# Optimization experiments

Hardware: AMD Instinct MI355X
Metric: run time of the kernel (lower is better)

Reference implementation:

```python
import jax, jax.numpy as jnp
import numpy as np

RES = 32            # input grid resolution
OUT_RES = 64        # after subdivide
C = 128             # channels (== out_channels -> skip is identity)
G = 32              # group-norm groups
N = 8192            # active input voxels
EPS = 1e-5

# 8 child offsets for subdivide, 27 stencil offsets for 3x3x3 submanifold conv
_OFFS8 = np.stack(np.meshgrid([0, 1], [0, 1], [0, 1], indexing='ij'), -1).reshape(-1, 3).astype(np.int32)
_OFFS27 = np.stack(np.meshgrid([-1, 0, 1], [-1, 0, 1], [-1, 0, 1], indexing='ij'), -1).reshape(-1, 3).astype(np.int32)


def group_norm(x, gamma, beta, num_groups=G, eps=EPS):
    # sparse group norm over all active voxels of the (single) sample
    n, c = x.shape
    xg = x.reshape(n, num_groups, c // num_groups)
    mean = xg.mean(axis=(0, 2), keepdims=True)
    var = xg.var(axis=(0, 2), keepdims=True)
    xn = (xg - mean) * jax.lax.rsqrt(var + eps)
    return xn.reshape(n, c) * gamma + beta


def subdivide_coords(coords):
    offs = jnp.asarray(_OFFS8)
    return (coords[:, None, :] * 2 + offs[None, :, :]).reshape(-1, 3)  # [8N, 3]


def subm_conv3d(feats, coords, W, b, grid_res):
    # submanifold 3x3x3 sparse conv: outputs only at active sites
    n = feats.shape[0]
    grid = jnp.full((grid_res, grid_res, grid_res), -1, dtype=jnp.int32)
    grid = grid.at[coords[:, 0], coords[:, 1], coords[:, 2]].set(
        jnp.arange(n, dtype=jnp.int32))
    out = jnp.zeros((n, W.shape[-1]), dtype=feats.dtype)
    for k in range(27):  # fixed small stencil loop
        off = jnp.asarray(_OFFS27[k])
        nb = coords + off
        inb = jnp.all((nb >= 0) & (nb < grid_res), axis=1)
        nbc = jnp.clip(nb, 0, grid_res - 1)
        idx = grid[nbc[:, 0], nbc[:, 1], nbc[:, 2]]
        mask = inb & (idx >= 0)
        g = jnp.where(mask[:, None], feats[jnp.where(mask, idx, 0)], 0.0)
        out = out + g @ W[k]
    return out + b


def setup_inputs() -> dict:
    key = jax.random.key(0)
    ks = jax.random.split(key, 8)
    rng = np.random.default_rng(0)
    flat = rng.choice(RES ** 3, size=N, replace=False)
    coords = np.stack([flat // (RES * RES), (flat // RES) % RES, flat % RES],
                      axis=-1).astype(np.int32)
    feats = jax.random.normal(ks[0], (N, C), dtype=jnp.float32)
    gamma1 = 1.0 + 0.1 * jax.random.normal(ks[1], (C,), dtype=jnp.float32)
    beta1 = 0.1 * jax.random.normal(ks[2], (C,), dtype=jnp.float32)
    W1 = jax.random.normal(ks[3], (27, C, C), dtype=jnp.float32) * 0.05
    b1 = jax.random.normal(ks[4], (C,), dtype=jnp.float32) * 0.05
    gamma2 = 1.0 + 0.1 * jax.random.normal(ks[5], (C,), dtype=jnp.float32)
    beta2 = 0.1 * jax.random.normal(ks[6], (C,), dtype=jnp.float32)
    W2 = jax.random.normal(ks[7], (27, C, C), dtype=jnp.float32) * 0.05
    b2 = jax.random.normal(jax.random.fold_in(key, 99), (C,), dtype=jnp.float32) * 0.05
    return {"feats": feats, "gamma1": gamma1, "beta1": beta1, "W1": W1,
            "b1": b1, "gamma2": gamma2, "beta2": beta2, "W2": W2, "b2": b2,
            "coords": jnp.asarray(coords)}


def reference(feats, gamma1, beta1, W1, b1, gamma2, beta2, W2, b2, coords):
    # act_layers: GroupNorm + SiLU at input resolution
    h = jax.nn.silu(group_norm(feats, gamma1, beta1))
    # subdivide both branch and residual (8 children per voxel)
    new_coords = subdivide_coords(coords)          # [8N, 3] in OUT_RES grid
    h = jnp.repeat(h, 8, axis=0)
    x_sub = jnp.repeat(feats, 8, axis=0)
    # out_layers: conv3 -> GN -> SiLU -> conv3 (submanifold, same active set)
    h = subm_conv3d(h, new_coords, W1, b1, OUT_RES)
    h = jax.nn.silu(group_norm(h, gamma2, beta2))
    h = subm_conv3d(h, new_coords, W2, b2, OUT_RES)
    # skip_connection is Identity since out_channels == channels
    return h + x_sub
```

## Files before the change

### kernel.cpp

```cpp
#include <hip/hip_runtime.h>

#define NPAR   8192
#define NCH    65536
#define RES    32
#define EPS    1e-5f

typedef __attribute__((ext_vector_type(8))) short short8;
typedef __attribute__((ext_vector_type(4))) float floatx4;

__device__ __forceinline__ unsigned short f2bf(float f) {
    union { float f; unsigned u; } v; v.f = f;
    unsigned r = v.u + 0x7fffu + ((v.u >> 16) & 1u);
    return (unsigned short)(r >> 16);
}
__device__ __forceinline__ float bf2f(unsigned short b) {
    union { unsigned u; float f; } v; v.u = ((unsigned)b) << 16;
    return v.f;
}
__device__ __forceinline__ void glds16(const void* g, void* l) {
    __builtin_amdgcn_global_load_lds(
        (__attribute__((address_space(1))) const void*)g,
        (__attribute__((address_space(3))) void*)l, 16, 0, 0);
}
__device__ __forceinline__ int k27_of(int o, int s) {
    return (((o >> 2) & 1) + ((s >> 2) & 1)) * 9 +
           (((o >> 1) & 1) + ((s >> 1) & 1)) * 3 +
           ((o & 1) + (s & 1));
}
__device__ __forceinline__ void axis_dlist(int o, int s, int* d, int& n) {
    if (o == 0) { if (s == 0) { d[0] = -1; n = 1; } else { d[0] = 0; d[1] = 1; n = 2; } }
    else        { if (s == 0) { d[0] = -1; d[1] = 0; n = 2; } else { d[0] = 1; n = 1; } }
}

__global__ void scatter_kernel(const int* __restrict__ coords, int* __restrict__ grid32,
                               float* __restrict__ stats, float* __restrict__ zpage) {
    int t = threadIdx.x;
    if (blockIdx.x == 0) {
        if (t < 128) stats[t] = 0.0f;
        else zpage[t - 128] = 0.0f;
    }
    int p = blockIdx.x * 256 + t;
    if (p < NPAR)
        grid32[(coords[p*3] << 10) + (coords[p*3+1] << 5) + coords[p*3+2]] = p;
}

__global__ void prep_kernel(const int* __restrict__ coords, const int* __restrict__ grid32,
                            int* __restrict__ idx_tab, int* __restrict__ pidx27,
                            const float* __restrict__ W1, const float* __restrict__ W2,
                            unsigned short* __restrict__ Wc1f, unsigned short* __restrict__ Wp2) {
    int b = blockIdx.x;
    if (b < 256) {
        int R = b * 256 + threadIdx.x;
        int p = R >> 3, o = R & 7;
        int bx = 2 * coords[p*3]   + ((o >> 2) & 1);
        int by = 2 * coords[p*3+1] + ((o >> 1) & 1);
        int bz = 2 * coords[p*3+2] + (o & 1);
#pragma unroll 1
        for (int k = 0; k < 27; ++k) {
            int fx = bx + k / 9 - 1, fy = by + (k / 3) % 3 - 1, fz = bz + k % 3 - 1;
            int src = -1;
            if ((unsigned)fx < 64u && (unsigned)fy < 64u && (unsigned)fz < 64u) {
                int r = grid32[((fx >> 1) << 10) + ((fy >> 1) << 5) + (fz >> 1)];
                if ((unsigned)r < (unsigned)NPAR)
                    src = r * 8 + ((fx & 1) << 2) + ((fy & 1) << 1) + (fz & 1);
            }
            idx_tab[k * NCH + R] = src;
        }
    } else if (b < 472) {
        int rem = (b - 256) * 256 + threadIdx.x;
        int lane = rem & 63;
        int ks   = (rem >> 6) & 3;
        int nb   = (rem >> 8) & 7;
        int tap  = rem >> 11;
        int n  = nb * 16 + (lane & 15);
        int k0 = ks * 32 + (lane >> 4) * 8;
        unsigned short v[8];
#pragma unroll
        for (int j = 0; j < 8; ++j) v[j] = f2bf(W2[tap * 16384 + (k0 + j) * 128 + n]);
        uint4 pk;
        pk.x = (unsigned)v[0] | ((unsigned)v[1] << 16);
        pk.y = (unsigned)v[2] | ((unsigned)v[3] << 16);
        pk.z = (unsigned)v[4] | ((unsigned)v[5] << 16);
        pk.w = (unsigned)v[6] | ((unsigned)v[7] << 16);
        *(uint4*)&Wp2[(long)rem * 8] = pk;
    } else if (b < 984) {
        int rem = (b - 472) * 256 + threadIdx.x;
        int lane  = rem & 63;
        int ks    = (rem >> 6) & 3;
        int nb    = (rem >> 8) & 7;
        int combo = rem >> 11;
        int o = combo >> 3, s = combo & 7;
        int n  = nb * 16 + (lane & 15);
        int k0 = ks * 32 + (lane >> 4) * 8;
        int d0[2], d1[2], d2[2], n0, n1, n2;
        axis_dlist((o >> 2) & 1, (s >> 2) & 1, d0, n0);
        axis_dlist((o >> 1) & 1, (s >> 1) & 1, d1, n1);
        axis_dlist(o & 1,        s & 1,        d2, n2);
        unsigned short v[8];
#pragma unroll
        for (int j = 0; j < 8; ++j) {
            float acc = 0.0f;
            for (int a = 0; a < n0; ++a)
                for (int bb = 0; bb < n1; ++bb)
                    for (int cc = 0; cc < n2; ++cc) {
                        int kk = (d0[a] + 1) * 9 + (d1[bb] + 1) * 3 + (d2[cc] + 1);
                        acc += W1[kk * 16384 + (k0 + j) * 128 + n];
                    }
            v[j] = f2bf(acc);
        }
        uint4 pk;
        pk.x = (unsigned)v[0] | ((unsigned)v[1] << 16);
        pk.y = (unsigned)v[2] | ((unsigned)v[3] << 16);
        pk.z = (unsigned)v[4] | ((unsigned)v[5] << 16);
        pk.w = (unsigned)v[6] | ((unsigned)v[7] << 16);
        *(uint4*)&Wc1f[(long)rem * 8] = pk;
    } else {
        int gid = (b - 984) * 256 + threadIdx.x;
        int k = gid >> 13, p = gid & 8191;
        int nx = coords[p*3]   + k / 9 - 1;
        int ny = coords[p*3+1] + (k / 3) % 3 - 1;
        int nz = coords[p*3+2] + k % 3 - 1;
        int src = -1;
        if ((unsigned)nx < 32u && (unsigned)ny < 32u && (unsigned)nz < 32u) {
            int r = grid32[(nx << 10) + (ny << 5) + nz];
            if ((unsigned)r < (unsigned)NPAR) src = r;
        }
        pidx27[k * NPAR + p] = src;
    }
}

__global__ void gn_stats_kernel(const float* __restrict__ x, float* __restrict__ sum,
                                float* __restrict__ sq, int nrows) {
    __shared__ float s_sum[32], s_sq[32];
    int t = threadIdx.x;
    if (t < 32) { s_sum[t] = 0.0f; s_sq[t] = 0.0f; }
    __syncthreads();
    const float4* x4 = (const float4*)x;
    int total = nrows * 32;
    int idx0 = blockIdx.x * blockDim.x + t;
    int g = idx0 & 31;
    float ls = 0.0f, lq = 0.0f;
    for (int idx = idx0; idx < total; idx += gridDim.x * blockDim.x) {
        float4 v = x4[idx];
        ls += v.x + v.y + v.z + v.w;
        lq += v.x * v.x + v.y * v.y + v.z * v.z + v.w * v.w;
    }
    atomicAdd(&s_sum[g], ls);
    atomicAdd(&s_sq[g], lq);
    __syncthreads();
    if (t < 32) { atomicAdd(&sum[t], s_sum[t]); atomicAdd(&sq[t], s_sq[t]); }
}

__global__ void gn_apply_kernel(const float* __restrict__ x, const float* __restrict__ sum,
                                const float* __restrict__ sq, const float* __restrict__ gamma,
                                const float* __restrict__ beta, unsigned short* __restrict__ y,
                                int nrows) {
    const float4* x4 = (const float4*)x;
    uint2* y2 = (uint2*)y;
    const float4* g4 = (const float4*)gamma;
    const float4* b4 = (const float4*)beta;
    float cnt = (float)nrows * 4.0f;
    int total = nrows * 32;
    for (int idx = blockIdx.x * blockDim.x + threadIdx.x; idx < total;
         idx += gridDim.x * blockDim.x) {
        int c4 = idx & 31;
        float mean = sum[c4] / cnt;
        float var = sq[c4] / cnt - mean * mean;
        float rstd = rsqrtf(var + EPS);
        float4 v = x4[idx];
        float4 gm = g4[c4];
        float4 bt = b4[c4];
        float a[4] = {v.x, v.y, v.z, v.w};
        float gg[4] = {gm.x, gm.y, gm.z, gm.w};
        float bb[4] = {bt.x, bt.y, bt.z, bt.w};
        unsigned short o[4];
#pragma unroll
        for (int i = 0; i < 4; ++i) {
            float tv = (a[i] - mean) * rstd * gg[i] + bb[i];
            o[i] = f2bf(tv / (1.0f + __expf(-tv)));
        }
        uint2 pk;
        pk.x = (unsigned)o[0] | ((unsigned)o[1] << 16);
        pk.y = (unsigned)o[2] | ((unsigned)o[3] << 16);
        y2[idx] = pk;
    }
}

__global__ void gn_apply_bf16_kernel(unsigned short* __restrict__ x,
                                     const float* __restrict__ sum, const float* __restrict__ sq,
                                     const float* __restrict__ gamma, const float* __restrict__ beta,
                                     int nrows) {
    uint2* x2 = (uint2*)x;
    const float4* g4 = (const float4*)gamma;
    const float4* b4 = (const float4*)beta;
    float cnt = (float)nrows * 4.0f;
    int total = nrows * 32;
    for (int idx = blockIdx.x * blockDim.x + threadIdx.x; idx < total;
         idx += gridDim.x * blockDim.x) {
        int c4 = idx & 31;
        float mean = sum[c4] / cnt;
        float var = sq[c4] / cnt - mean * mean;
        float rstd = rsqrtf(var + EPS);
        uint2 pk = x2[idx];
        float a[4] = {bf2f((unsigned short)(pk.x & 0xffff)), bf2f((unsigned short)(pk.x >> 16)),
                      bf2f((unsigned short)(pk.y & 0xffff)), bf2f((unsigned short)(pk.y >> 16))};
        float4 gm = g4[c4];
        float4 bt = b4[c4];
        float gg[4] = {gm.x, gm.y, gm.z, gm.w};
        float bb[4] = {bt.x, bt.y, bt.z, bt.w};
        unsigned short o[4];
#pragma unroll
        for (int i = 0; i < 4; ++i) {
            float tv = (a[i] - mean) * rstd * gg[i] + bb[i];
            o[i] = f2bf(tv / (1.0f + __expf(-tv)));
        }
        pk.x = (unsigned)o[0] | ((unsigned)o[1] << 16);
        pk.y = (unsigned)o[2] | ((unsigned)o[3] << 16);
        x2[idx] = pk;
    }
}

__global__ void __launch_bounds__(256) conv1_fold_kernel(
    const unsigned short* __restrict__ Ag, const unsigned short* __restrict__ Wc1f,
    const float* __restrict__ bias, const int* __restrict__ pidx27,
    unsigned short* __restrict__ outp, const float* __restrict__ zpage,
    float* __restrict__ gsum, float* __restrict__ gsq) {
    __shared__ unsigned short A_lds[2][16384];

    int t = threadIdx.x;
    int o  = blockIdx.x & 7;
    int P0 = (blockIdx.x >> 3) << 7;
    const unsigned short* Wb = Wc1f + ((long)o << 17);
    int wv = t >> 6, lane = t & 63, quad = lane >> 4, l16 = lane & 15;
    int wm = wv & 1, wn = wv >> 1;
    int r16 = lane >> 2, cch = lane & 3;
    int c0 = wv * 2, c1 = wv * 2 + 1;
    int row0 = ((c0 >> 2) << 6) + ((c0 & 3) << 4) + r16;
    int row1 = ((c1 >> 2) << 6) + ((c1 & 3) << 4) + r16;
    int base0 = ((c0 >> 2) << 13) + ((c0 & 3) << 11);
    int base1 = ((c1 >> 2) << 13) + ((c1 & 3) << 11);
    const unsigned short* zsrc = (const unsigned short*)zpage;

    floatx4 acc[4][4];
#pragma unroll
    for (int mt = 0; mt < 4; ++mt)
#pragma unroll
        for (int nt = 0; nt < 4; ++nt)
            acc[mt][nt] = (floatx4){0.f, 0.f, 0.f, 0.f};

    int iv0 = pidx27[k27_of(o, 0) * NPAR + P0 + row0];
    int iv1 = pidx27[k27_of(o, 0) * NPAR + P0 + row1];
    {
        const unsigned short* g0 = (iv0 >= 0) ? Ag + (long)iv0 * 128 : zsrc;
        const unsigned short* g1 = (iv1 >= 0) ? Ag + (long)iv1 * 128 : zsrc;
#pragma unroll
        for (int i = 0; i < 4; ++i) glds16(g0 + i * 32 + cch * 8, &A_lds[0][base0 + i * 512]);
#pragma unroll
        for (int i = 0; i < 4; ++i) glds16(g1 + i * 32 + cch * 8, &A_lds[0][base1 + i * 512]);
    }
    int nv0 = pidx27[k27_of(o, 1) * NPAR + P0 + row0];
    int nv1 = pidx27[k27_of(o, 1) * NPAR + P0 + row1];
    __syncthreads();

#pragma unroll 1
    for (int s = 0; s < 8; ++s) {
        int cur = s & 1;
        if (s < 7) {
            const unsigned short* g0 = (nv0 >= 0) ? Ag + (long)nv0 * 128 : zsrc;
            const unsigned short* g1 = (nv1 >= 0) ? Ag + (long)nv1 * 128 : zsrc;
#pragma unroll
            for (int i = 0; i < 4; ++i) glds16(g0 + i * 32 + cch * 8, &A_lds[1 - cur][base0 + i * 512]);
#pragma unroll
            for (int i = 0; i < 4; ++i) glds16(g1 + i * 32 + cch * 8, &A_lds[1 - cur][base1 + i * 512]);
            if (s < 6) {
                nv0 = pidx27[k27_of(o, s + 2) * NPAR + P0 + row0];
                nv1 = pidx27[k27_of(o, s + 2) * NPAR + P0 + row1];
            }
        }
#pragma unroll
        for (int ks = 0; ks < 4; ++ks) {
            short8 afr[4], bfr[4];
#pragma unroll
            for (int mt = 0; mt < 4; ++mt)
                afr[mt] = *(const short8*)&A_lds[cur][(wm << 13) + (mt << 11) + (ks << 9) + (l16 << 5) + (quad << 3)];
#pragma unroll
            for (int nt = 0; nt < 4; ++nt) {
                int cb = wn * 4 + nt;
                bfr[nt] = *(const short8*)&Wb[((((s << 3) + cb) << 2) + ks) * 512 + (lane << 3)];
            }
#pragma unroll
            for (int mt = 0; mt < 4; ++mt)
#pragma unroll
                for (int nt = 0; nt < 4; ++nt)
                    acc[mt][nt] = __builtin_amdgcn_mfma_f32_16x16x32_bf16(
                        afr[mt], bfr[nt], acc[mt][nt], 0, 0, 0);
        }
        __syncthreads();
    }

    float s_[4] = {0.f, 0.f, 0.f, 0.f}, q_[4] = {0.f, 0.f, 0.f, 0.f};
#pragma unroll
    for (int nt = 0; nt < 4; ++nt) {
        int col = wn * 64 + nt * 16 + l16;
        float bv = bias[col];
#pragma unroll
        for (int mt = 0; mt < 4; ++mt) {
#pragma unroll
            for (int r = 0; r < 4; ++r) {
                int prow = wm * 64 + mt * 16 + quad * 4 + r;
                long R = ((long)(P0 + prow) << 3) + o;
                float v = acc[mt][nt][r] + bv;
                unsigned short u = f2bf(v);
                outp[R * 128 + col] = u;
                float vr = bf2f(u);
                s_[nt] += vr;
                q_[nt] += vr * vr;
            }
        }
    }
    float* sred = (float*)A_lds;
    if (t < 64) sred[t] = 0.0f;
    __syncthreads();
#pragma unroll
    for (int nt = 0; nt < 4; ++nt) {
        int g = (wn * 64 + nt * 16 + l16) >> 2;
        atomicAdd(&sred[g], s_[nt]);
        atomicAdd(&sred[32 + g], q_[nt]);
    }
    __syncthreads();
    if (t < 32) { atomicAdd(&gsum[t], sred[t]); atomicAdd(&gsq[t], sred[32 + t]); }
}

__global__ void __launch_bounds__(256) conv2_kernel(
    const unsigned short* __restrict__ Ag, const unsigned short* __restrict__ Wp,
    const float* __restrict__ bias, const int* __restrict__ idx_tab,
    const float* __restrict__ resid, float* __restrict__ outp,
    const float* __restrict__ zpage) {
    __shared__ unsigned short A_lds[2][16384];

    int t = threadIdx.x;
    int R0 = blockIdx.x * 128;
    int wv = t >> 6, lane = t & 63, quad = lane >> 4, l16 = lane & 15;
    int wm = wv & 1, wn = wv >> 1;
    int r16 = lane >> 2, cch = lane & 3;
    int c0 = wv * 2, c1 = wv * 2 + 1;
    int row0 = ((c0 >> 2) << 6) + ((c0 & 3) << 4) + r16;
    int row1 = ((c1 >> 2) << 6) + ((c1 & 3) << 4) + r16;
    int base0 = ((c0 >> 2) << 13) + ((c0 & 3) << 11);
    int base1 = ((c1 >> 2) << 13) + ((c1 & 3) << 11);
    const unsigned short* zsrc = (const unsigned short*)zpage;

    floatx4 acc[4][4];
#pragma unroll
    for (int mt = 0; mt < 4; ++mt)
#pragma unroll
        for (int nt = 0; nt < 4; ++nt)
            acc[mt][nt] = (floatx4){0.f, 0.f, 0.f, 0.f};

    int iv0 = idx_tab[R0 + row0], iv1 = idx_tab[R0 + row1];
    {
        const unsigned short* g0 = (iv0 >= 0) ? Ag + (long)iv0 * 128 : zsrc;
        const unsigned short* g1 = (iv1 >= 0) ? Ag + (long)iv1 * 128 : zsrc;
#pragma unroll
        for (int i = 0; i < 4; ++i) glds16(g0 + i * 32 + cch * 8, &A_lds[0][base0 + i * 512]);
#pragma unroll
        for (int i = 0; i < 4; ++i) glds16(g1 + i * 32 + cch * 8, &A_lds[0][base1 + i * 512]);
    }
    int nv0 = idx_tab[NCH + R0 + row0], nv1 = idx_tab[NCH + R0 + row1];
    __syncthreads();

#pragma unroll 1
    for (int k = 0; k < 27; ++k) {
        int cur = k & 1;
        if (k < 26) {
            const unsigned short* g0 = (nv0 >= 0) ? Ag + (long)nv0 * 128 : zsrc;
            const unsigned short* g1 = (nv1 >= 0) ? Ag + (long)nv1 * 128 : zsrc;
#pragma unroll
            for (int i = 0; i < 4; ++i) glds16(g0 + i * 32 + cch * 8, &A_lds[1 - cur][base0 + i * 512]);
#pragma unroll
            for (int i = 0; i < 4; ++i) glds16(g1 + i * 32 + cch * 8, &A_lds[1 - cur][base1 + i * 512]);
            if (k < 25) {
                nv0 = idx_tab[(k + 2) * NCH + R0 + row0];
                nv1 = idx_tab[(k + 2) * NCH + R0 + row1];
            }
        }
#pragma unroll
        for (int ks = 0; ks < 4; ++ks) {
            short8 afr[4], bfr[4];
#pragma unroll
            for (int mt = 0; mt < 4; ++mt)
                afr[mt] = *(const short8*)&A_lds[cur][(wm << 13) + (mt << 11) + (ks << 9) + (l16 << 5) + (quad << 3)];
#pragma unroll
            for (int nt = 0; nt < 4; ++nt) {
                int cb = wn * 4 + nt;
                bfr[nt] = *(const short8*)&Wp[((((k << 3) + cb) << 2) + ks) * 512 + (lane << 3)];
            }
#pragma unroll
            for (int mt = 0; mt < 4; ++mt)
#pragma unroll
                for (int nt = 0; nt < 4; ++nt)
                    acc[mt][nt] = __builtin_amdgcn_mfma_f32_16x16x32_bf16(
                        afr[mt], bfr[nt], acc[mt][nt], 0, 0, 0);
        }
        __syncthreads();
    }

#pragma unroll
    for (int nt = 0; nt < 4; ++nt) {
        int col = wn * 64 + nt * 16 + l16;
        float bv = bias[col];
#pragma unroll
        for (int mt = 0; mt < 4; ++mt) {
#pragma unroll
            for (int r = 0; r < 4; ++r) {
                int row = wm * 64 + mt * 16 + quad * 4 + r;
                long R = (long)R0 + row;
                float v = acc[mt][nt][r] + bv + resid[(R >> 3) * 128 + col];
                outp[R * 128 + col] = v;
            }
        }
    }
}

extern "C" void kernel_launch(void* const* d_in, const int* in_sizes, int n_in,
                              void* d_out, int out_size, void* d_ws, size_t ws_size,
                              hipStream_t stream) {
    const float* feats  = (const float*)d_in[0];
    const float* gamma1 = (const float*)d_in[1];
    const float* beta1  = (const float*)d_in[2];
    const float* W1     = (const float*)d_in[3];
    const float* b1     = (const float*)d_in[4];
    const float* gamma2 = (const float*)d_in[5];
    const float* beta2  = (const float*)d_in[6];
    const float* W2     = (const float*)d_in[7];
    const float* b2     = (const float*)d_in[8];
    const int*   coords = (const int*)d_in[9];
    float* out = (float*)d_out;

    char* ws = (char*)d_ws;
    unsigned short* h0b  = (unsigned short*)(ws);
    unsigned short* h1b  = (unsigned short*)(ws + (2u << 20));
    unsigned short* Wc1f = (unsigned short*)(ws + (18u << 20));
    unsigned short* Wp2  = (unsigned short*)(ws + (20u << 20));
    int*   grid32        = (int*)  (ws + (21u << 20));
    float* stats         = (float*)(ws + (21u << 20) + 131072);
    float* zpage         = (float*)(ws + (21u << 20) + 131072 + 512);
    int*   idx_tab       = (int*)  (ws + (22u << 20));
    int*   pidx27        = (int*)  (ws + (30u << 20));

    scatter_kernel<<<NPAR / 256, 256, 0, stream>>>(coords, grid32, stats, zpage);
    prep_kernel<<<1848, 256, 0, stream>>>(coords, grid32, idx_tab, pidx27,
                                          W1, W2, Wc1f, Wp2);

    gn_stats_kernel<<<256, 256, 0, stream>>>(feats, stats + 0, stats + 32, NPAR);
    gn_apply_kernel<<<256, 256, 0, stream>>>(feats, stats + 0, stats + 32, gamma1, beta1, h0b, NPAR);

    conv1_fold_kernel<<<8 * (NPAR / 128), 256, 0, stream>>>(h0b, Wc1f, b1, pidx27,
                                                            h1b, zpage,
                                                            stats + 64, stats + 96);

    gn_apply_bf16_kernel<<<512, 256, 0, stream>>>(h1b, stats + 64, stats + 96, gamma2, beta2, NCH);

    conv2_kernel<<<NCH / 128, 256, 0, stream>>>(h1b, Wp2, b2, idx_tab,
                                                feats, out, zpage);
}
```

Before: 214.9 us.

## Merge scatter/GN-stats and prep/GN-apply launches; reorder subdivided rows child-major

Folds the first group-norm statistics pass into the grid-scatter kernel and the group-norm apply pass into the table/weight prep kernel, cutting the pipeline from four launches to two plus a memset. Stats and zero page are now cleared with hipMemsetAsync instead of inside the scatter kernel. The layout of the subdivided feature rows changes from parent-major (p*8+o) to child-major (o*NPAR+p), with conv1 output and the conv2 gather table updated to match. The layout change alters memory access patterns in conv1 stores and conv2 gathers, and any code not shown that assumes the old ordering would break correctness.

```diff
diff --git a/kernel.cpp b/kernel.cpp
--- a/kernel.cpp
+++ b/kernel.cpp
@@ -32,22 +32,42 @@
     else        { if (s == 0) { d[0] = -1; d[1] = 0; n = 2; } else { d[0] = 1; n = 1; } }
 }
 
-__global__ void scatter_kernel(const int* __restrict__ coords, int* __restrict__ grid32,
-                               float* __restrict__ stats, float* __restrict__ zpage) {
+__global__ void k1_kernel(const int* __restrict__ coords, int* __restrict__ grid32,
+                          const float* __restrict__ x, float* __restrict__ sum,
+                          float* __restrict__ sq) {
+    int b = blockIdx.x;
     int t = threadIdx.x;
-    if (blockIdx.x == 0) {
-        if (t < 128) stats[t] = 0.0f;
-        else zpage[t - 128] = 0.0f;
-    }
-    int p = blockIdx.x * 256 + t;
-    if (p < NPAR)
+    if (b < 32) {
+        int p = b * 256 + t;
         grid32[(coords[p*3] << 10) + (coords[p*3+1] << 5) + coords[p*3+2]] = p;
-}
-
-__global__ void prep_kernel(const int* __restrict__ coords, const int* __restrict__ grid32,
-                            int* __restrict__ idx_tab, int* __restrict__ pidx27,
-                            const float* __restrict__ W1, const float* __restrict__ W2,
-                            unsigned short* __restrict__ Wc1f, unsigned short* __restrict__ Wp2) {
+    } else {
+        __shared__ float s_sum[32], s_sq[32];
+        if (t < 32) { s_sum[t] = 0.0f; s_sq[t] = 0.0f; }
+        __syncthreads();
+        const float4* x4 = (const float4*)x;
+        int total = NPAR * 32;
+        int idx0 = (b - 32) * 256 + t;
+        int g = idx0 & 31;
+        float ls = 0.0f, lq = 0.0f;
+        for (int idx = idx0; idx < total; idx += 256 * 256) {
+            float4 v = x4[idx];
+            ls += v.x + v.y + v.z + v.w;
+            lq += v.x * v.x + v.y * v.y + v.z * v.z + v.w * v.w;
+        }
+        atomicAdd(&s_sum[g], ls);
+        atomicAdd(&s_sq[g], lq);
+        __syncthreads();
+        if (t < 32) { atomicAdd(&sum[t], s_sum[t]); atomicAdd(&sq[t], s_sq[t]); }
+    }
+}
+
+__global__ void k2_kernel(const int* __restrict__ coords, const int* __restrict__ grid32,
+                          int* __restrict__ idx_tab, int* __restrict__ pidx27,
+                          const float* __restrict__ W1, const float* __restrict__ W2,
+                          unsigned short* __restrict__ Wc1f, unsigned short* __restrict__ Wp2,
+                          const float* __restrict__ x, const float* __restrict__ sum,
+                          const float* __restrict__ sq, const float* __restrict__ gamma,
+                          const float* __restrict__ beta, unsigned short* __restrict__ y) {
     int b = blockIdx.x;
     if (b < 256) {
         int R = b * 256 + threadIdx.x;
@@ -62,7 +82,7 @@
             if ((unsigned)fx < 64u && (unsigned)fy < 64u && (unsigned)fz < 64u) {
                 int r = grid32[((fx >> 1) << 10) + ((fy >> 1) << 5) + (fz >> 1)];
                 if ((unsigned)r < (unsigned)NPAR)
-                    src = r * 8 + ((fx & 1) << 2) + ((fy & 1) << 1) + (fz & 1);
+                    src = (((fx & 1) << 2) + ((fy & 1) << 1) + (fz & 1)) * NPAR + r;
             }
             idx_tab[k * NCH + R] = src;
         }
@@ -114,7 +134,7 @@
         pk.z = (unsigned)v[4] | ((unsigned)v[5] << 16);
         pk.w = (unsigned)v[6] | ((unsigned)v[7] << 16);
         *(uint4*)&Wc1f[(long)rem * 8] = pk;
-    } else {
+    } else if (b < 1848) {
         int gid = (b - 984) * 256 + threadIdx.x;
         int k = gid >> 13, p = gid & 8191;
         int nx = coords[p*3]   + k / 9 - 1;
@@ -126,63 +146,35 @@
             if ((unsigned)r < (unsigned)NPAR) src = r;
         }
         pidx27[k * NPAR + p] = src;
-    }
-}
-
-__global__ void gn_stats_kernel(const float* __restrict__ x, float* __restrict__ sum,
-                                float* __restrict__ sq, int nrows) {
-    __shared__ float s_sum[32], s_sq[32];
-    int t = threadIdx.x;
-    if (t < 32) { s_sum[t] = 0.0f; s_sq[t] = 0.0f; }
-    __syncthreads();
-    const float4* x4 = (const float4*)x;
-    int total = nrows * 32;
-    int idx0 = blockIdx.x * blockDim.x + t;
-    int g = idx0 & 31;
-    float ls = 0.0f, lq = 0.0f;
-    for (int idx = idx0; idx < total; idx += gridDim.x * blockDim.x) {
-        float4 v = x4[idx];
-        ls += v.x + v.y + v.z + v.w;
-        lq += v.x * v.x + v.y * v.y + v.z * v.z + v.w * v.w;
-    }
-    atomicAdd(&s_sum[g], ls);
-    atomicAdd(&s_sq[g], lq);
-    __syncthreads();
-    if (t < 32) { atomicAdd(&sum[t], s_sum[t]); atomicAdd(&sq[t], s_sq[t]); }
-}
-
-__global__ void gn_apply_kernel(const float* __restrict__ x, const float* __restrict__ sum,
-                                const float* __restrict__ sq, const float* __restrict__ gamma,
-                                const float* __restrict__ beta, unsigned short* __restrict__ y,
-                                int nrows) {
-    const float4* x4 = (const float4*)x;
-    uint2* y2 = (uint2*)y;
-    const float4* g4 = (const float4*)gamma;
-    const float4* b4 = (const float4*)beta;
-    float cnt = (float)nrows * 4.0f;
-    int total = nrows * 32;
-    for (int idx = blockIdx.x * blockDim.x + threadIdx.x; idx < total;
-         idx += gridDim.x * blockDim.x) {
-        int c4 = idx & 31;
-        float mean = sum[c4] / cnt;
-        float var = sq[c4] / cnt - mean * mean;
-        float rstd = rsqrtf(var + EPS);
-        float4 v = x4[idx];
-        float4 gm = g4[c4];
-        float4 bt = b4[c4];
-        float a[4] = {v.x, v.y, v.z, v.w};
-        float gg[4] = {gm.x, gm.y, gm.z, gm.w};
-        float bb[4] = {bt.x, bt.y, bt.z, bt.w};
-        unsigned short o[4];
-#pragma unroll
-        for (int i = 0; i < 4; ++i) {
-            float tv = (a[i] - mean) * rstd * gg[i] + bb[i];
-            o[i] = f2bf(tv / (1.0f + __expf(-tv)));
-        }
-        uint2 pk;
-        pk.x = (unsigned)o[0] | ((unsigned)o[1] << 16);
-        pk.y = (unsigned)o[2] | ((unsigned)o[3] << 16);
-        y2[idx] = pk;
+    } else {
+        const float4* x4 = (const float4*)x;
+        uint2* y2 = (uint2*)y;
+        const float4* g4 = (const float4*)gamma;
+        const float4* b4 = (const float4*)beta;
+        float cnt = (float)NPAR * 4.0f;
+        int total = NPAR * 32;
+        for (int idx = (b - 1848) * 256 + threadIdx.x; idx < total; idx += 256 * 256) {
+            int c4 = idx & 31;
+            float mean = sum[c4] / cnt;
+            float var = sq[c4] / cnt - mean * mean;
+            float rstd = rsqrtf(var + EPS);
+            float4 v = x4[idx];
+            float4 gm = g4[c4];
+            float4 bt = b4[c4];
+            float a[4] = {v.x, v.y, v.z, v.w};
+            float gg[4] = {gm.x, gm.y, gm.z, gm.w};
+            float bb[4] = {bt.x, bt.y, bt.z, bt.w};
+            unsigned short o[4];
+#pragma unroll
+            for (int i = 0; i < 4; ++i) {
+                float tv = (a[i] - mean) * rstd * gg[i] + bb[i];
+                o[i] = f2bf(tv / (1.0f + __expf(-tv)));
+            }
+            uint2 pk;
+            pk.x = (unsigned)o[0] | ((unsigned)o[1] << 16);
+            pk.y = (unsigned)o[2] | ((unsigned)o[3] << 16);
+            y2[idx] = pk;
+        }
     }
 }
 
@@ -308,7 +300,7 @@
 #pragma unroll
             for (int r = 0; r < 4; ++r) {
                 int prow = wm * 64 + mt * 16 + quad * 4 + r;
-                long R = ((long)(P0 + prow) << 3) + o;
+                long R = (long)o * NPAR + P0 + prow;
                 float v = acc[mt][nt][r] + bv;
                 unsigned short u = f2bf(v);
                 outp[R * 128 + col] = u;
@@ -448,12 +440,12 @@
     int*   idx_tab       = (int*)  (ws + (22u << 20));
     int*   pidx27        = (int*)  (ws + (30u << 20));
 
-    scatter_kernel<<<NPAR / 256, 256, 0, stream>>>(coords, grid32, stats, zpage);
-    prep_kernel<<<1848, 256, 0, stream>>>(coords, grid32, idx_tab, pidx27,
-                                          W1, W2, Wc1f, Wp2);
-
-    gn_stats_kernel<<<256, 256, 0, stream>>>(feats, stats + 0, stats + 32, NPAR);
-    gn_apply_kernel<<<256, 256, 0, stream>>>(feats, stats + 0, stats + 32, gamma1, beta1, h0b, NPAR);
+    hipMemsetAsync(stats, 0, 1024, stream);
+
+    k1_kernel<<<288, 256, 0, stream>>>(coords, grid32, feats, stats + 0, stats + 32);
+    k2_kernel<<<2104, 256, 0, stream>>>(coords, grid32, idx_tab, pidx27,
+                                        W1, W2, Wc1f, Wp2,
+                                        feats, stats + 0, stats + 32, gamma1, beta1, h0b);
 
     conv1_fold_kernel<<<8 * (NPAR / 128), 256, 0, stream>>>(h0b, Wc1f, b1, pidx27,
                                                             h1b, zpage,
```

New measurement: 211.7 us. Within noise of the previous version (-1.5%).
